# Kernel tuning notes

Measured on AMD Instinct MI355X. Metric: run time of the kernel, lower is better.

Reference implementation:

```python
import jax, jax.numpy as jnp
import numpy as np

B, N, L = 4, 16, 2048
E = 32768
CH = (64, 128, 128, 128)
EPS = 1e-5


def setup_inputs() -> dict:
    key = jax.random.key(0)
    ks = jax.random.split(key, 6)
    x = jax.random.normal(ks[0], (B, N, CH[0], L), jnp.float32)
    edge_index = jax.random.randint(ks[1], (2, E), 0, L, dtype=jnp.int64)

    def xavier(k, fi, fo):
        std = (2.0 / (fi + fo)) ** 0.5
        return jax.random.normal(k, (fi, fo), jnp.float32) * std

    W1 = xavier(ks[2], CH[0], CH[1])
    W2 = xavier(ks[3], 2 * CH[1], CH[2])
    W3 = xavier(ks[4], 2 * CH[2], CH[3])
    return dict(
        x=x, edge_index=edge_index,
        W1=W1, b1=jnp.zeros((CH[1],), jnp.float32),
        W2=W2, b2=jnp.zeros((CH[2],), jnp.float32),
        W3=W3, b3=jnp.zeros((CH[3],), jnp.float32),
        g1=jnp.ones((2 * CH[1],), jnp.float32), be1=jnp.zeros((2 * CH[1],), jnp.float32),
        g2=jnp.ones((2 * CH[2],), jnp.float32), be2=jnp.zeros((2 * CH[2],), jnp.float32),
        g3=jnp.ones((2 * CH[3],), jnp.float32), be3=jnp.zeros((2 * CH[3],), jnp.float32),
    )


def _gcn_norm(edge_index, l):
    # PyG gcn_norm with improved=True: self loops get weight 2, sym normalization
    src, dst = edge_index[0], edge_index[1]
    loop = jnp.arange(l)
    src_f = jnp.concatenate([src, loop])
    dst_f = jnp.concatenate([dst, loop])
    w = jnp.concatenate([jnp.ones((src.shape[0],), jnp.float32),
                         2.0 * jnp.ones((l,), jnp.float32)])
    deg = jax.ops.segment_sum(w, dst_f, num_segments=l)
    dinv = jnp.where(deg > 0, jax.lax.rsqrt(deg), 0.0)
    return src_f, dst_f, dinv[src_f] * w * dinv[dst_f]


def _gcn(h, W, bias, src, dst, norm):
    # h: [G, l, c_in] -> [G, l, c_out];  out[i] = sum_{j->i} norm_ij * (h_j @ W) + b
    hW = jnp.einsum('glc,cf->glf', h, W)
    msg = hW[:, src, :] * norm[None, :, None]
    out = jnp.zeros_like(hW).at[:, dst, :].add(msg)
    return out + bias


def _block(h, W, bias, g, beta, src, dst, norm, b, n, l):
    # h: [b, n, l, c_in]
    a = _gcn(h.reshape(b * n, l, h.shape[-1]), W, bias, src, dst, norm)
    a = a.reshape(b, n, l, -1)
    amax = a.max(axis=1, keepdims=True)
    a = jnp.concatenate([a, jnp.broadcast_to(amax, a.shape)], axis=-1)  # [b,n,l,2c]
    # BatchNorm1d training stats over (b, n, l) per channel (biased var)
    mean = a.mean(axis=(0, 1, 2))
    var = a.var(axis=(0, 1, 2))
    return jax.nn.relu((a - mean) * jax.lax.rsqrt(var + EPS) * g + beta)


def reference(x, edge_index, W1, b1, W2, b2, W3, b3, g1, be1, g2, be2, g3, be3):
    b, n, c, l = x.shape
    h = jnp.transpose(x, (0, 1, 3, 2))  # [b, n, l, c] node-major
    src, dst, norm = _gcn_norm(edge_index, l)
    h = _block(h, W1, b1, g1, be1, src, dst, norm, b, n, l)
    h = _block(h, W2, b2, g2, be2, src, dst, norm, b, n, l)
    h = _block(h, W3, b3, g3, be3, src, dst, norm, b, n, l)
    # match torch output layout [b*n, 2*channels[3], l]
    return jnp.transpose(h.reshape(b * n, l, -1), (0, 2, 1))
```

## Files before the change

### kernel.cpp

```cpp
#include <hip/hip_runtime.h>
#include <hip/hip_bf16.h>
#include <cstddef>
#include <cstdint>

#define BB 4
#define NN 16
#define GG 64
#define LL 2048
#define EE 32768
#define EF (EE + LL)
#define C0 64
#define CC 256
#define EPS 1e-5f

typedef __bf16 bf16x8 __attribute__((ext_vector_type(8)));
typedef __bf16 bf16x4 __attribute__((ext_vector_type(4)));
typedef __bf16 bf16x2 __attribute__((ext_vector_type(2)));
typedef float f32x4 __attribute__((ext_vector_type(4)));

struct __align__(8) Edge { int col; float val; };


__global__ void detect_kernel(const int* __restrict__ ei, int* __restrict__ flag) {
    int t = threadIdx.x;
    int bad = 0;
    for (int i = t; i < 256; i += 64) bad |= (ei[2 * i + 1] != 0) ? 1 : 0;
    int any = __any(bad);
    if (t == 0) *flag = any ? 0 : 1;
}

__global__ void prep_init_kernel(const void* __restrict__ ei, const int* __restrict__ flag,
                                 int* __restrict__ e32, float* __restrict__ deg,
                                 int* __restrict__ cnt, float* __restrict__ sums) {
    int i = blockIdx.x * 256 + threadIdx.x;
    if (i < 2 * EE) {
        int v;
        if (*flag)
            v = (int)((const long long*)ei)[i];
        else
            v = ((const int*)ei)[i];
        e32[i] = v;
    }
    if (i < LL) { deg[i] = 2.0f; cnt[i] = 1; }
    if (i < 512) sums[i] = 0.0f;
}

__global__ void deg_kernel(const int* __restrict__ e32, float* __restrict__ deg,
                           int* __restrict__ cnt) {
    int e = blockIdx.x * 256 + threadIdx.x;
    if (e >= EE) return;
    int d = e32[EE + e];
    atomicAdd(&deg[d], 1.0f);
    atomicAdd(&cnt[d], 1);
}

__global__ void scan_dinv_kernel(const int* __restrict__ cnt, const float* __restrict__ deg,
                                 int* __restrict__ rowptr, int* __restrict__ cursor,
                                 float* __restrict__ dinv) {
    __shared__ int part[256];
    int t = threadIdx.x;
    int base = t * 8;
    int loc[8];
    int s = 0;
#pragma unroll
    for (int j = 0; j < 8; ++j) {
        loc[j] = s; s += cnt[base + j];
        dinv[base + j] = rsqrtf(deg[base + j]);
    }
    part[t] = s;
    __syncthreads();
    if (t == 0) {
        int run = 0;
        for (int i = 0; i < 256; ++i) { int v = part[i]; part[i] = run; run += v; }
    }
    __syncthreads();
    int off = part[t];
#pragma unroll
    for (int j = 0; j < 8; ++j) {
        int rp = off + loc[j];
        rowptr[base + j] = rp;
        cursor[base + j] = rp;
    }
    if (t == 255) rowptr[LL] = off + s;
}

__global__ void fill_kernel(const int* __restrict__ e32, const float* __restrict__ dinv,
                            int* __restrict__ cursor, Edge* __restrict__ edges) {
    int idx = blockIdx.x * 256 + threadIdx.x;
    if (idx >= EF) return;
    int s, d; float w;
    if (idx < EE) {
        s = e32[idx]; d = e32[EE + idx];
        w = dinv[s] * dinv[d];
    } else {
        int i = idx - EE;
        s = i; d = i;
        w = 2.0f * dinv[i] * dinv[i];
    }
    int pos = atomicAdd(&cursor[d], 1);
    edges[pos].col = s;
    edges[pos].val = w;
}


__global__ void prep_w_all(const float* __restrict__ W0, const float* __restrict__ W1,
                           const float* __restrict__ W2, __bf16* __restrict__ Wf0,
                           __bf16* __restrict__ Wf1, __bf16* __restrict__ Wf2) {
    int t = blockIdx.x * 256 + threadIdx.x;
    const float* W; __bf16* Wf;
    if (t < 1024)      { W = W0; Wf = Wf0; }
    else if (t < 5120) { W = W1; Wf = Wf1; t -= 1024; }
    else if (t < 9216) { W = W2; Wf = Wf2; t -= 5120; }
    else return;
    int lane = t & 63;
    int rest = t >> 6;
    int n16 = rest & 7;
    int ks = rest >> 3;
    int col = n16 * 16 + (lane & 15);
    int k0 = ks * 32 + (lane >> 4) * 8;
    bf16x8 v;
#pragma unroll
    for (int j = 0; j < 8; ++j) v[j] = (__bf16)W[(size_t)(k0 + j) * 128 + col];
    *(bf16x8*)(Wf + (size_t)t * 8) = v;
}


__global__ void transpose_x(const float* __restrict__ x, float* __restrict__ h) {
    __shared__ float t[32][33];
    int g = blockIdx.z, c0 = blockIdx.y * 32, l0 = blockIdx.x * 32;
    int tx = threadIdx.x, ty = threadIdx.y;
    const float* xp = x + ((size_t)g * C0 + c0) * LL + l0;
#pragma unroll
    for (int i = ty; i < 32; i += 8) t[i][tx] = xp[(size_t)i * LL + tx];
    __syncthreads();
    float* hp = h + ((size_t)g * LL + l0) * C0 + c0;
#pragma unroll
    for (int i = ty; i < 32; i += 8) hp[(size_t)i * C0 + tx] = t[tx][i];
}


template <int K, bool BN>
__global__ __launch_bounds__(256) void gemm_mfma(const float* __restrict__ A0,
                                                 const float* __restrict__ amax,
                                                 const float* __restrict__ scb,
                                                 const __bf16* __restrict__ Wf,
                                                 __bf16* __restrict__ hw) {
    const int g = blockIdx.y;
    const int l0 = blockIdx.x * 64;
    const int tid = threadIdx.x;
    const int wid = tid >> 6;
    const int lane = tid & 63;
    __shared__ __align__(16) __bf16 As[64 * 64];

    f32x4 acc[8];
#pragma unroll
    for (int nf = 0; nf < 8; ++nf) acc[nf] = (f32x4){0.f, 0.f, 0.f, 0.f};

    for (int kt = 0; kt < K / 64; ++kt) {
#pragma unroll
        for (int it = 0; it < 4; ++it) {
            int f4 = tid + it * 256;
            int row = f4 >> 4;
            int kq = (f4 & 15) * 4;
            int gk = kt * 64 + kq;
            float4 v;
            if constexpr (BN) {
                if (gk < 128)
                    v = *(const float4*)(A0 + ((size_t)g * LL + l0 + row) * 128 + gk);
                else
                    v = *(const float4*)(amax + ((size_t)(g >> 4) * LL + l0 + row) * 128 + (gk - 128));
                float4 s = *(const float4*)(scb + gk);
                float4 b = *(const float4*)(scb + 256 + gk);
                v.x = fmaxf(fmaf(v.x, s.x, b.x), 0.f);
                v.y = fmaxf(fmaf(v.y, s.y, b.y), 0.f);
                v.z = fmaxf(fmaf(v.z, s.z, b.z), 0.f);
                v.w = fmaxf(fmaf(v.w, s.w, b.w), 0.f);
            } else {
                v = *(const float4*)(A0 + ((size_t)g * LL + l0 + row) * 64 + gk);
            }
            int sidx = row * 64 + (kq ^ ((row & 7) << 3));
            bf16x4 pv = {(__bf16)v.x, (__bf16)v.y, (__bf16)v.z, (__bf16)v.w};
            *(bf16x4*)(&As[sidx]) = pv;
        }
        __syncthreads();
#pragma unroll
        for (int ks2 = 0; ks2 < 2; ++ks2) {
            const int row = wid * 16 + (lane & 15);
            const int kk = ks2 * 32 + (lane >> 4) * 8;
            bf16x8 af = *(const bf16x8*)(&As[row * 64 + (kk ^ ((row & 7) << 3))]);
            const int ksg = kt * 2 + ks2;
            const __bf16* wp = Wf + (size_t)ksg * 8 * 512 + lane * 8;
#pragma unroll
            for (int nf = 0; nf < 8; ++nf) {
                bf16x8 bfr = *(const bf16x8*)(wp + nf * 512);
                acc[nf] = __builtin_amdgcn_mfma_f32_16x16x32_bf16(af, bfr, acc[nf], 0, 0, 0);
            }
        }
        __syncthreads();
    }
    __bf16* op = hw + ((size_t)g * LL + l0) * 128;
#pragma unroll
    for (int nf = 0; nf < 8; ++nf) {
        int col = nf * 16 + (lane & 15);
#pragma unroll
        for (int j = 0; j < 4; ++j) {
            int row = wid * 16 + (lane >> 4) * 4 + j;
            op[(size_t)row * 128 + col] = (__bf16)acc[nf][j];
        }
    }
}


__global__ __launch_bounds__(256) void agg_kernel(const __bf16* __restrict__ hw,
                                                  const float* __restrict__ bias,
                                                  const int* __restrict__ rowptr,
                                                  const Edge* __restrict__ edges,
                                                  float* __restrict__ aout) {
    const int lane = threadIdx.x & 63;
    const int grp = lane >> 4;
    const int ch16 = lane & 15;
    const int bid = blockIdx.x;
    const int xcd = bid & 7;
    const int slot = bid >> 3;
    const int gswz = ((slot >> 9) << 3) + xcd;
    const int within = slot & 511;
    int node = (gswz << 11) + within * 4 + (threadIdx.x >> 6);
    node = __builtin_amdgcn_readfirstlane(node);
    const int g = node >> 11, l = node & (LL - 1);
    const __bf16* __restrict__ base = hw + (size_t)g * LL * 128 + ch16 * 8;
    const int j0 = rowptr[l];
    const int deg = rowptr[l + 1] - j0;

    float acc[8];
#pragma unroll
    for (int j = 0; j < 8; ++j) acc[j] = 0.0f;

    for (int d0 = 0; d0 < deg; d0 += 64) {
        const int cnt = min(64, deg - d0);
        Edge e;
        e.col = 0; e.val = 0.0f;
        if (lane < cnt) e = edges[j0 + d0 + lane];
        int d = 0;
        for (; d + 8 <= cnt; d += 8) {
            int i1 = d + grp, i2 = d + 4 + grp;
            int c1 = __shfl(e.col, i1); float w1 = __shfl(e.val, i1);
            int c2 = __shfl(e.col, i2); float w2 = __shfl(e.val, i2);
            bf16x8 v1 = *(const bf16x8*)(base + (size_t)c1 * 128);
            bf16x8 v2 = *(const bf16x8*)(base + (size_t)c2 * 128);
#pragma unroll
            for (int j = 0; j < 8; ++j) acc[j] = fmaf(w1, (float)v1[j], acc[j]);
#pragma unroll
            for (int j = 0; j < 8; ++j) acc[j] = fmaf(w2, (float)v2[j], acc[j]);
        }
        for (; d < cnt; d += 4) {
            int i1 = d + grp;
            int c1 = __shfl(e.col, i1); float w1 = __shfl(e.val, i1);
            bf16x8 v1 = *(const bf16x8*)(base + (size_t)c1 * 128);
#pragma unroll
            for (int j = 0; j < 8; ++j) acc[j] = fmaf(w1, (float)v1[j], acc[j]);
        }
    }
#pragma unroll
    for (int j = 0; j < 8; ++j) {
        acc[j] += __shfl_xor(acc[j], 16);
        acc[j] += __shfl_xor(acc[j], 32);
    }
    if (grp == 0) {
        float4 b0 = *(const float4*)(bias + ch16 * 8);
        float4 b1 = *(const float4*)(bias + ch16 * 8 + 4);
        float4 s0 = make_float4(acc[0] + b0.x, acc[1] + b0.y, acc[2] + b0.z, acc[3] + b0.w);
        float4 s1 = make_float4(acc[4] + b1.x, acc[5] + b1.y, acc[6] + b1.z, acc[7] + b1.w);
        float* op = aout + (size_t)node * 128 + ch16 * 8;
        *(float4*)op = s0;
        *(float4*)(op + 4) = s1;
    }
}


__global__ void maxstats_kernel(const float* __restrict__ a, float* __restrict__ amax,
                                float* __restrict__ sums, float* __restrict__ sumsq) {
    int bb = blockIdx.x >> 7;
    int lt = blockIdx.x & 127;
    int l0 = lt * 16;
    int f = threadIdx.x;
    float s = 0.f, ss = 0.f, sa = 0.f, ssa = 0.f;
    for (int li = 0; li < 16; ++li) {
        int l = l0 + li;
        float m = -3.402823466e38f;
#pragma unroll
        for (int n = 0; n < NN; ++n) {
            float v = a[(((size_t)(bb * NN + n) * LL + l) * 128) + f];
            m = fmaxf(m, v);
            s += v;
            ss = fmaf(v, v, ss);
        }
        amax[((size_t)bb * LL + l) * 128 + f] = m;
        sa += m;
        ssa = fmaf(m, m, ssa);
    }
    atomicAdd(&sums[f], s);
    atomicAdd(&sumsq[f], ss);
    atomicAdd(&sums[128 + f], sa);
    atomicAdd(&sumsq[128 + f], ssa);
}

__global__ void bnfinal_kernel(float* __restrict__ sums, float* __restrict__ sumsq,
                               const float* __restrict__ gamma, const float* __restrict__ beta,
                               float* __restrict__ scb) {
    int f = threadIdx.x;
    float cntv = (f < 128) ? (float)(BB * NN * LL) : (float)(BB * LL);
    float mean = sums[f] / cntv;
    float var = sumsq[f] / cntv - mean * mean;
    float s = gamma[f] * rsqrtf(var + EPS);
    scb[f] = s;
    scb[256 + f] = beta[f] - mean * s;
    sums[f] = 0.0f;
    sumsq[f] = 0.0f;
}


__global__ void transpose_norm_out(const float* __restrict__ a, const float* __restrict__ amax,
                                   const float* __restrict__ scb, float* __restrict__ out) {
    __shared__ float t[64][65];
    int g = blockIdx.z, f0 = blockIdx.y * 64, l0 = blockIdx.x * 64;
    int tx = threadIdx.x, ty = threadIdx.y;
    int f = f0 + tx;
    float s = scb[f], b = scb[256 + f];
#pragma unroll
    for (int i = ty; i < 64; i += 8) {
        int l = l0 + i;
        float v;
        if (f0 < 128)
            v = a[((size_t)g * LL + l) * 128 + f];
        else
            v = amax[((size_t)(g >> 4) * LL + l) * 128 + (f - 128)];
        t[i][tx] = fmaxf(fmaf(v, s, b), 0.f);
    }
    __syncthreads();
    float* op = out + ((size_t)g * CC + f0) * LL + l0;
#pragma unroll
    for (int i = ty; i < 64; i += 8) op[(size_t)i * LL + tx] = t[tx][i];
}


extern "C" void kernel_launch(void* const* d_in, const int* in_sizes, int n_in,
                              void* d_out, int out_size, void* d_ws, size_t ws_size,
                              hipStream_t stream) {
    const float* x = (const float*)d_in[0];
    const void* ei = d_in[1];
    const float* W[3] = {(const float*)d_in[2], (const float*)d_in[4], (const float*)d_in[6]};
    const float* bia[3] = {(const float*)d_in[3], (const float*)d_in[5], (const float*)d_in[7]};
    const float* gam[3] = {(const float*)d_in[8], (const float*)d_in[10], (const float*)d_in[12]};
    const float* bet[3] = {(const float*)d_in[9], (const float*)d_in[11], (const float*)d_in[13]};
    float* out = (float*)d_out;

    char* w = (char*)d_ws;
    float* h0   = (float*)w;  w += (size_t)GG * LL * C0 * 4;
    float* a    = (float*)w;  w += (size_t)GG * LL * 128 * 4;
    __bf16* hw  = (__bf16*)w; w += (size_t)GG * LL * 128 * 2;
    float* amax = (float*)w;  w += (size_t)BB * LL * 128 * 4;
    __bf16* Wf[3];
    Wf[0] = (__bf16*)w; w += 65536 * 2;
    Wf[1] = (__bf16*)w; w += 65536 * 2;
    Wf[2] = (__bf16*)w; w += 65536 * 2;
    int*   e32   = (int*)w;    w += (size_t)2 * EE * 4;
    float* deg   = (float*)w;  w += LL * 4;
    int*   cnt   = (int*)w;    w += LL * 4;
    int*   rowptr= (int*)w;    w += (LL + 4) * 4;
    int*   cursor= (int*)w;    w += LL * 4;
    Edge*  edges = (Edge*)w;   w += (size_t)EF * 8;
    float* dinv  = (float*)w;  w += LL * 4;
    float* sums  = (float*)w;  w += 256 * 4;
    float* sumsq = (float*)w;  w += 256 * 4;
    float* scb   = (float*)w;  w += 512 * 4;
    int*   flag  = (int*)w;    w += 256;

    detect_kernel<<<1, 64, 0, stream>>>((const int*)ei, flag);
    prep_init_kernel<<<(2 * EE + 255) / 256, 256, 0, stream>>>(ei, flag, e32, deg, cnt, sums);
    deg_kernel<<<(EE + 255) / 256, 256, 0, stream>>>(e32, deg, cnt);
    scan_dinv_kernel<<<1, 256, 0, stream>>>(cnt, deg, rowptr, cursor, dinv);
    fill_kernel<<<(EF + 255) / 256, 256, 0, stream>>>(e32, dinv, cursor, edges);

    prep_w_all<<<36, 256, 0, stream>>>(W[0], W[1], W[2], Wf[0], Wf[1], Wf[2]);

    transpose_x<<<dim3(LL / 32, C0 / 32, GG), dim3(32, 8), 0, stream>>>(x, h0);

    gemm_mfma<64, false><<<dim3(LL / 64, GG), 256, 0, stream>>>(h0, amax, scb, Wf[0], hw);
    agg_kernel<<<GG * LL / 4, 256, 0, stream>>>(hw, bia[0], rowptr, edges, a);
    maxstats_kernel<<<BB * (LL / 16), 128, 0, stream>>>(a, amax, sums, sumsq);
    bnfinal_kernel<<<1, 256, 0, stream>>>(sums, sumsq, gam[0], bet[0], scb);

    gemm_mfma<256, true><<<dim3(LL / 64, GG), 256, 0, stream>>>(a, amax, scb, Wf[1], hw);
    agg_kernel<<<GG * LL / 4, 256, 0, stream>>>(hw, bia[1], rowptr, edges, a);
    maxstats_kernel<<<BB * (LL / 16), 128, 0, stream>>>(a, amax, sums, sumsq);
    bnfinal_kernel<<<1, 256, 0, stream>>>(sums, sumsq, gam[1], bet[1], scb);

    gemm_mfma<256, true><<<dim3(LL / 64, GG), 256, 0, stream>>>(a, amax, scb, Wf[2], hw);
    agg_kernel<<<GG * LL / 4, 256, 0, stream>>>(hw, bia[2], rowptr, edges, a);
    maxstats_kernel<<<BB * (LL / 16), 128, 0, stream>>>(a, amax, sums, sumsq);
    bnfinal_kernel<<<1, 256, 0, stream>>>(sums, sumsq, gam[2], bet[2], scb);

    transpose_norm_out<<<dim3(LL / 64, CC / 64, GG), dim3(64, 8), 0, stream>>>(a, amax, scb, out);
}
```

Before: 531.6 us.

## Store activations in bf16, fuse transpose into GEMM and BN finalize into stats

Intermediate activations and the per-batch max tensor are now stored in bf16 instead of fp32, roughly halving the memory traffic of the aggregation, stats, GEMM and output kernels. The input transpose is folded into the first GEMM's tile load, and the BatchNorm finalize step moves into the stats kernel using a last-block ticket. Edge conversion and degree counting are merged into one kernel, and the init and detect kernels are merged into another. The GEMM epilogue is staged through shared memory for vectorized stores, and the aggregation loop unrolls to four edges per step. Rounding to bf16 before max and BN statistics adds precision loss, and the ticket scheme depends on atomics and fences being correct.

```diff
diff --git a/kernel.cpp b/kernel.cpp
--- a/kernel.cpp
+++ b/kernel.cpp
@@ -21,35 +21,37 @@
 struct __align__(8) Edge { int col; float val; };
 
 
-__global__ void detect_kernel(const int* __restrict__ ei, int* __restrict__ flag) {
-    int t = threadIdx.x;
-    int bad = 0;
-    for (int i = t; i < 256; i += 64) bad |= (ei[2 * i + 1] != 0) ? 1 : 0;
-    int any = __any(bad);
-    if (t == 0) *flag = any ? 0 : 1;
-}
-
-__global__ void prep_init_kernel(const void* __restrict__ ei, const int* __restrict__ flag,
-                                 int* __restrict__ e32, float* __restrict__ deg,
-                                 int* __restrict__ cnt, float* __restrict__ sums) {
+__global__ void detect_init_kernel(const int* __restrict__ ei, int* __restrict__ flag,
+                                   float* __restrict__ deg, int* __restrict__ cnt,
+                                   float* __restrict__ gstats, int* __restrict__ ticket) {
     int i = blockIdx.x * 256 + threadIdx.x;
-    if (i < 2 * EE) {
-        int v;
-        if (*flag)
-            v = (int)((const long long*)ei)[i];
-        else
-            v = ((const int*)ei)[i];
-        e32[i] = v;
-    }
     if (i < LL) { deg[i] = 2.0f; cnt[i] = 1; }
-    if (i < 512) sums[i] = 0.0f;
-}
-
-__global__ void deg_kernel(const int* __restrict__ e32, float* __restrict__ deg,
-                           int* __restrict__ cnt) {
+    if (i < 4096) gstats[i] = 0.0f;
+    if (i == 0) *ticket = 0;
+    if (blockIdx.x == 0 && threadIdx.x < 64) {
+        int t = threadIdx.x;
+        int bad = 0;
+        for (int k = t; k < 256; k += 64) bad |= (ei[2 * k + 1] != 0) ? 1 : 0;
+        int any = __any(bad);
+        if (t == 0) *flag = any ? 0 : 1;
+    }
+}
+
+__global__ void conv_deg_kernel(const void* __restrict__ ei, const int* __restrict__ flag,
+                                int* __restrict__ e32, float* __restrict__ deg,
+                                int* __restrict__ cnt) {
     int e = blockIdx.x * 256 + threadIdx.x;
     if (e >= EE) return;
-    int d = e32[EE + e];
+    int s, d;
+    if (*flag) {
+        s = (int)((const long long*)ei)[e];
+        d = (int)((const long long*)ei)[EE + e];
+    } else {
+        s = ((const int*)ei)[e];
+        d = ((const int*)ei)[EE + e];
+    }
+    e32[e] = s;
+    e32[EE + e] = d;
     atomicAdd(&deg[d], 1.0f);
     atomicAdd(&cnt[d], 1);
 }
@@ -125,23 +127,9 @@
 }
 
 
-__global__ void transpose_x(const float* __restrict__ x, float* __restrict__ h) {
-    __shared__ float t[32][33];
-    int g = blockIdx.z, c0 = blockIdx.y * 32, l0 = blockIdx.x * 32;
-    int tx = threadIdx.x, ty = threadIdx.y;
-    const float* xp = x + ((size_t)g * C0 + c0) * LL + l0;
-#pragma unroll
-    for (int i = ty; i < 32; i += 8) t[i][tx] = xp[(size_t)i * LL + tx];
-    __syncthreads();
-    float* hp = h + ((size_t)g * LL + l0) * C0 + c0;
-#pragma unroll
-    for (int i = ty; i < 32; i += 8) hp[(size_t)i * C0 + tx] = t[tx][i];
-}
-
-
 template <int K, bool BN>
-__global__ __launch_bounds__(256) void gemm_mfma(const float* __restrict__ A0,
-                                                 const float* __restrict__ amax,
+__global__ __launch_bounds__(256) void gemm_mfma(const void* __restrict__ A0v,
+                                                 const __bf16* __restrict__ amax,
                                                  const float* __restrict__ scb,
                                                  const __bf16* __restrict__ Wf,
                                                  __bf16* __restrict__ hw) {
@@ -150,37 +138,54 @@
     const int tid = threadIdx.x;
     const int wid = tid >> 6;
     const int lane = tid & 63;
-    __shared__ __align__(16) __bf16 As[64 * 64];
+    __shared__ __align__(16) float smem[64 * 132];
+    __bf16* As = (__bf16*)smem;
 
     f32x4 acc[8];
 #pragma unroll
     for (int nf = 0; nf < 8; ++nf) acc[nf] = (f32x4){0.f, 0.f, 0.f, 0.f};
 
     for (int kt = 0; kt < K / 64; ++kt) {
-#pragma unroll
-        for (int it = 0; it < 4; ++it) {
-            int f4 = tid + it * 256;
-            int row = f4 >> 4;
-            int kq = (f4 & 15) * 4;
-            int gk = kt * 64 + kq;
-            float4 v;
-            if constexpr (BN) {
+        if constexpr (!BN) {
+            const float* x = (const float*)A0v;
+            const int l = tid & 63, cq = tid >> 6;
+#pragma unroll
+            for (int it = 0; it < 4; ++it) {
+                int cbase = it * 16 + cq * 4;
+                bf16x4 pv;
+#pragma unroll
+                for (int j = 0; j < 4; ++j)
+                    pv[j] = (__bf16)x[((size_t)g * C0 + cbase + j) * LL + l0 + l];
+                *(bf16x4*)(&As[l * 64 + (cbase ^ ((l & 7) << 3))]) = pv;
+            }
+        } else {
+            const __bf16* a = (const __bf16*)A0v;
+#pragma unroll
+            for (int it = 0; it < 2; ++it) {
+                int f8 = tid + it * 256;
+                int row = f8 >> 3;
+                int oct = f8 & 7;
+                int gk = kt * 64 + oct * 8;
+                bf16x8 v;
                 if (gk < 128)
-                    v = *(const float4*)(A0 + ((size_t)g * LL + l0 + row) * 128 + gk);
+                    v = *(const bf16x8*)(a + ((size_t)g * LL + l0 + row) * 128 + gk);
                 else
-                    v = *(const float4*)(amax + ((size_t)(g >> 4) * LL + l0 + row) * 128 + (gk - 128));
-                float4 s = *(const float4*)(scb + gk);
-                float4 b = *(const float4*)(scb + 256 + gk);
-                v.x = fmaxf(fmaf(v.x, s.x, b.x), 0.f);
-                v.y = fmaxf(fmaf(v.y, s.y, b.y), 0.f);
-                v.z = fmaxf(fmaf(v.z, s.z, b.z), 0.f);
-                v.w = fmaxf(fmaf(v.w, s.w, b.w), 0.f);
-            } else {
-                v = *(const float4*)(A0 + ((size_t)g * LL + l0 + row) * 64 + gk);
+                    v = *(const bf16x8*)(amax + ((size_t)(g >> 4) * LL + l0 + row) * 128 + (gk - 128));
+                float4 s0 = *(const float4*)(scb + gk);
+                float4 s1 = *(const float4*)(scb + gk + 4);
+                float4 b0 = *(const float4*)(scb + 256 + gk);
+                float4 b1 = *(const float4*)(scb + 256 + gk + 4);
+                bf16x8 pv;
+                pv[0] = (__bf16)fmaxf(fmaf((float)v[0], s0.x, b0.x), 0.f);
+                pv[1] = (__bf16)fmaxf(fmaf((float)v[1], s0.y, b0.y), 0.f);
+                pv[2] = (__bf16)fmaxf(fmaf((float)v[2], s0.z, b0.z), 0.f);
+                pv[3] = (__bf16)fmaxf(fmaf((float)v[3], s0.w, b0.w), 0.f);
+                pv[4] = (__bf16)fmaxf(fmaf((float)v[4], s1.x, b1.x), 0.f);
+                pv[5] = (__bf16)fmaxf(fmaf((float)v[5], s1.y, b1.y), 0.f);
+                pv[6] = (__bf16)fmaxf(fmaf((float)v[6], s1.z, b1.z), 0.f);
+                pv[7] = (__bf16)fmaxf(fmaf((float)v[7], s1.w, b1.w), 0.f);
+                *(bf16x8*)(&As[row * 64 + ((oct * 8) ^ ((row & 7) << 3))]) = pv;
             }
-            int sidx = row * 64 + (kq ^ ((row & 7) << 3));
-            bf16x4 pv = {(__bf16)v.x, (__bf16)v.y, (__bf16)v.z, (__bf16)v.w};
-            *(bf16x4*)(&As[sidx]) = pv;
         }
         __syncthreads();
 #pragma unroll
@@ -198,15 +203,25 @@
         }
         __syncthreads();
     }
-    __bf16* op = hw + ((size_t)g * LL + l0) * 128;
 #pragma unroll
     for (int nf = 0; nf < 8; ++nf) {
         int col = nf * 16 + (lane & 15);
 #pragma unroll
         for (int j = 0; j < 4; ++j) {
             int row = wid * 16 + (lane >> 4) * 4 + j;
-            op[(size_t)row * 128 + col] = (__bf16)acc[nf][j];
-        }
+            smem[row * 132 + col] = acc[nf][j];
+        }
+    }
+    __syncthreads();
+    const int row = tid >> 2, seg = tid & 3;
+    __bf16* dst = hw + ((size_t)g * LL + l0 + row) * 128 + seg * 32;
+    const float* src = smem + row * 132 + seg * 32;
+#pragma unroll
+    for (int q = 0; q < 4; ++q) {
+        bf16x8 o;
+#pragma unroll
+        for (int i = 0; i < 8; ++i) o[i] = (__bf16)src[q * 8 + i];
+        *(bf16x8*)(dst + q * 8) = o;
     }
 }
 
@@ -215,7 +230,7 @@
                                                   const float* __restrict__ bias,
                                                   const int* __restrict__ rowptr,
                                                   const Edge* __restrict__ edges,
-                                                  float* __restrict__ aout) {
+                                                  __bf16* __restrict__ aout) {
     const int lane = threadIdx.x & 63;
     const int grp = lane >> 4;
     const int ch16 = lane & 15;
@@ -236,23 +251,31 @@
     for (int j = 0; j < 8; ++j) acc[j] = 0.0f;
 
     for (int d0 = 0; d0 < deg; d0 += 64) {
-        const int cnt = min(64, deg - d0);
+        const int cntE = min(64, deg - d0);
         Edge e;
         e.col = 0; e.val = 0.0f;
-        if (lane < cnt) e = edges[j0 + d0 + lane];
+        if (lane < cntE) e = edges[j0 + d0 + lane];
         int d = 0;
-        for (; d + 8 <= cnt; d += 8) {
-            int i1 = d + grp, i2 = d + 4 + grp;
+        for (; d + 16 <= cntE; d += 16) {
+            int i1 = d + grp, i2 = d + 4 + grp, i3 = d + 8 + grp, i4 = d + 12 + grp;
             int c1 = __shfl(e.col, i1); float w1 = __shfl(e.val, i1);
             int c2 = __shfl(e.col, i2); float w2 = __shfl(e.val, i2);
+            int c3 = __shfl(e.col, i3); float w3 = __shfl(e.val, i3);
+            int c4 = __shfl(e.col, i4); float w4 = __shfl(e.val, i4);
             bf16x8 v1 = *(const bf16x8*)(base + (size_t)c1 * 128);
             bf16x8 v2 = *(const bf16x8*)(base + (size_t)c2 * 128);
+            bf16x8 v3 = *(const bf16x8*)(base + (size_t)c3 * 128);
+            bf16x8 v4 = *(const bf16x8*)(base + (size_t)c4 * 128);
 #pragma unroll
             for (int j = 0; j < 8; ++j) acc[j] = fmaf(w1, (float)v1[j], acc[j]);
 #pragma unroll
             for (int j = 0; j < 8; ++j) acc[j] = fmaf(w2, (float)v2[j], acc[j]);
-        }
-        for (; d < cnt; d += 4) {
+#pragma unroll
+            for (int j = 0; j < 8; ++j) acc[j] = fmaf(w3, (float)v3[j], acc[j]);
+#pragma unroll
+            for (int j = 0; j < 8; ++j) acc[j] = fmaf(w4, (float)v4[j], acc[j]);
+        }
+        for (; d < cntE; d += 4) {
             int i1 = d + grp;
             int c1 = __shfl(e.col, i1); float w1 = __shfl(e.val, i1);
             bf16x8 v1 = *(const bf16x8*)(base + (size_t)c1 * 128);
@@ -268,58 +291,82 @@
     if (grp == 0) {
         float4 b0 = *(const float4*)(bias + ch16 * 8);
         float4 b1 = *(const float4*)(bias + ch16 * 8 + 4);
-        float4 s0 = make_float4(acc[0] + b0.x, acc[1] + b0.y, acc[2] + b0.z, acc[3] + b0.w);
-        float4 s1 = make_float4(acc[4] + b1.x, acc[5] + b1.y, acc[6] + b1.z, acc[7] + b1.w);
-        float* op = aout + (size_t)node * 128 + ch16 * 8;
-        *(float4*)op = s0;
-        *(float4*)(op + 4) = s1;
-    }
-}
-
-
-__global__ void maxstats_kernel(const float* __restrict__ a, float* __restrict__ amax,
-                                float* __restrict__ sums, float* __restrict__ sumsq) {
-    int bb = blockIdx.x >> 7;
-    int lt = blockIdx.x & 127;
-    int l0 = lt * 16;
-    int f = threadIdx.x;
-    float s = 0.f, ss = 0.f, sa = 0.f, ssa = 0.f;
-    for (int li = 0; li < 16; ++li) {
-        int l = l0 + li;
-        float m = -3.402823466e38f;
+        bf16x8 o;
+        o[0] = (__bf16)(acc[0] + b0.x); o[1] = (__bf16)(acc[1] + b0.y);
+        o[2] = (__bf16)(acc[2] + b0.z); o[3] = (__bf16)(acc[3] + b0.w);
+        o[4] = (__bf16)(acc[4] + b1.x); o[5] = (__bf16)(acc[5] + b1.y);
+        o[6] = (__bf16)(acc[6] + b1.z); o[7] = (__bf16)(acc[7] + b1.w);
+        *(bf16x8*)(aout + (size_t)node * 128 + ch16 * 8) = o;
+    }
+}
+
+
+__global__ __launch_bounds__(256) void maxstats_kernel(const __bf16* __restrict__ a,
+                                                       __bf16* __restrict__ amax,
+                                                       float* __restrict__ gstats,
+                                                       int* __restrict__ ticket,
+                                                       const float* __restrict__ gamma,
+                                                       const float* __restrict__ beta,
+                                                       float* __restrict__ scb) {
+    __shared__ float bl[512];
+    __shared__ int lastflag;
+    const int t = threadIdx.x;
+    bl[t] = 0.f; bl[256 + t] = 0.f;
+    __syncthreads();
+    const int bb = blockIdx.x >> 7;
+    const int lt = blockIdx.x & 127;
+    const int c2 = t & 63;
+    const int lq = t >> 6;
+    const int l0 = lt * 16 + lq * 4;
+    float sx = 0.f, sy = 0.f, qx = 0.f, qy = 0.f;
+    float sax = 0.f, say = 0.f, qax = 0.f, qay = 0.f;
+#pragma unroll
+    for (int i = 0; i < 4; ++i) {
+        int l = l0 + i;
+        float mx = -3.402823466e38f, my = -3.402823466e38f;
 #pragma unroll
         for (int n = 0; n < NN; ++n) {
-            float v = a[(((size_t)(bb * NN + n) * LL + l) * 128) + f];
-            m = fmaxf(m, v);
-            s += v;
-            ss = fmaf(v, v, ss);
-        }
-        amax[((size_t)bb * LL + l) * 128 + f] = m;
-        sa += m;
-        ssa = fmaf(m, m, ssa);
-    }
-    atomicAdd(&sums[f], s);
-    atomicAdd(&sumsq[f], ss);
-    atomicAdd(&sums[128 + f], sa);
-    atomicAdd(&sumsq[128 + f], ssa);
-}
-
-__global__ void bnfinal_kernel(float* __restrict__ sums, float* __restrict__ sumsq,
-                               const float* __restrict__ gamma, const float* __restrict__ beta,
-                               float* __restrict__ scb) {
-    int f = threadIdx.x;
-    float cntv = (f < 128) ? (float)(BB * NN * LL) : (float)(BB * LL);
-    float mean = sums[f] / cntv;
-    float var = sumsq[f] / cntv - mean * mean;
-    float s = gamma[f] * rsqrtf(var + EPS);
-    scb[f] = s;
-    scb[256 + f] = beta[f] - mean * s;
-    sums[f] = 0.0f;
-    sumsq[f] = 0.0f;
-}
-
-
-__global__ void transpose_norm_out(const float* __restrict__ a, const float* __restrict__ amax,
+            bf16x2 v = *(const bf16x2*)(a + ((size_t)(bb * NN + n) * LL + l) * 128 + c2 * 2);
+            float v0 = (float)v[0], v1 = (float)v[1];
+            mx = fmaxf(mx, v0); my = fmaxf(my, v1);
+            sx += v0; sy += v1;
+            qx = fmaf(v0, v0, qx); qy = fmaf(v1, v1, qy);
+        }
+        bf16x2 mv = {(__bf16)mx, (__bf16)my};
+        *(bf16x2*)(amax + ((size_t)bb * LL + l) * 128 + c2 * 2) = mv;
+        sax += mx; say += my;
+        qax = fmaf(mx, mx, qax); qay = fmaf(my, my, qay);
+    }
+    atomicAdd(&bl[c2 * 2], sx);        atomicAdd(&bl[c2 * 2 + 1], sy);
+    atomicAdd(&bl[128 + c2 * 2], sax); atomicAdd(&bl[128 + c2 * 2 + 1], say);
+    atomicAdd(&bl[256 + c2 * 2], qx);  atomicAdd(&bl[256 + c2 * 2 + 1], qy);
+    atomicAdd(&bl[384 + c2 * 2], qax); atomicAdd(&bl[384 + c2 * 2 + 1], qay);
+    __syncthreads();
+    const int slot = blockIdx.x & 7;
+    atomicAdd(&gstats[slot * 512 + t], bl[t]);
+    atomicAdd(&gstats[slot * 512 + 256 + t], bl[256 + t]);
+    __threadfence();
+    if (t == 0) lastflag = (atomicAdd(ticket, 1) == 511) ? 1 : 0;
+    __syncthreads();
+    if (lastflag) {
+        float sm = 0.f, sq = 0.f;
+#pragma unroll
+        for (int sl = 0; sl < 8; ++sl) {
+            sm += atomicExch(&gstats[sl * 512 + t], 0.f);
+            sq += atomicExch(&gstats[sl * 512 + 256 + t], 0.f);
+        }
+        float cntv = (t < 128) ? (float)(BB * NN * LL) : (float)(BB * LL);
+        float mean = sm / cntv;
+        float var = sq / cntv - mean * mean;
+        float sc = gamma[t] * rsqrtf(var + EPS);
+        scb[t] = sc;
+        scb[256 + t] = beta[t] - mean * sc;
+        if (t == 0) *ticket = 0;
+    }
+}
+
+
+__global__ void transpose_norm_out(const __bf16* __restrict__ a, const __bf16* __restrict__ amax,
                                    const float* __restrict__ scb, float* __restrict__ out) {
     __shared__ float t[64][65];
     int g = blockIdx.z, f0 = blockIdx.y * 64, l0 = blockIdx.x * 64;
@@ -331,9 +378,9 @@
         int l = l0 + i;
         float v;
         if (f0 < 128)
-            v = a[((size_t)g * LL + l) * 128 + f];
+            v = (float)a[((size_t)g * LL + l) * 128 + f];
         else
-            v = amax[((size_t)(g >> 4) * LL + l) * 128 + (f - 128)];
+            v = (float)amax[((size_t)(g >> 4) * LL + l) * 128 + (f - 128)];
         t[i][tx] = fmaxf(fmaf(v, s, b), 0.f);
     }
     __syncthreads();
@@ -355,50 +402,42 @@
     float* out = (float*)d_out;
 
     char* w = (char*)d_ws;
-    float* h0   = (float*)w;  w += (size_t)GG * LL * C0 * 4;
-    float* a    = (float*)w;  w += (size_t)GG * LL * 128 * 4;
-    __bf16* hw  = (__bf16*)w; w += (size_t)GG * LL * 128 * 2;
-    float* amax = (float*)w;  w += (size_t)BB * LL * 128 * 4;
+    __bf16* a_bf  = (__bf16*)w; w += (size_t)GG * LL * 128 * 2;
+    __bf16* hw    = (__bf16*)w; w += (size_t)GG * LL * 128 * 2;
+    __bf16* amax  = (__bf16*)w; w += (size_t)BB * LL * 128 * 2;
     __bf16* Wf[3];
     Wf[0] = (__bf16*)w; w += 65536 * 2;
     Wf[1] = (__bf16*)w; w += 65536 * 2;
     Wf[2] = (__bf16*)w; w += 65536 * 2;
-    int*   e32   = (int*)w;    w += (size_t)2 * EE * 4;
-    float* deg   = (float*)w;  w += LL * 4;
-    int*   cnt   = (int*)w;    w += LL * 4;
-    int*   rowptr= (int*)w;    w += (LL + 4) * 4;
-    int*   cursor= (int*)w;    w += LL * 4;
-    Edge*  edges = (Edge*)w;   w += (size_t)EF * 8;
-    float* dinv  = (float*)w;  w += LL * 4;
-    float* sums  = (float*)w;  w += 256 * 4;
-    float* sumsq = (float*)w;  w += 256 * 4;
-    float* scb   = (float*)w;  w += 512 * 4;
-    int*   flag  = (int*)w;    w += 256;
-
-    detect_kernel<<<1, 64, 0, stream>>>((const int*)ei, flag);
-    prep_init_kernel<<<(2 * EE + 255) / 256, 256, 0, stream>>>(ei, flag, e32, deg, cnt, sums);
-    deg_kernel<<<(EE + 255) / 256, 256, 0, stream>>>(e32, deg, cnt);
+    int*   e32    = (int*)w;    w += (size_t)2 * EE * 4;
+    float* deg    = (float*)w;  w += LL * 4;
+    int*   cnt    = (int*)w;    w += LL * 4;
+    int*   rowptr = (int*)w;    w += (LL + 4) * 4;
+    int*   cursor = (int*)w;    w += LL * 4;
+    Edge*  edges  = (Edge*)w;   w += (size_t)EF * 8;
+    float* dinv   = (float*)w;  w += LL * 4;
+    float* gstats = (float*)w;  w += 8 * 512 * 4;
+    float* scb    = (float*)w;  w += 512 * 4;
+    int*   flag   = (int*)w;    w += 256;
+    int*   ticket = (int*)w;    w += 256;
+
+    detect_init_kernel<<<16, 256, 0, stream>>>((const int*)ei, flag, deg, cnt, gstats, ticket);
+    conv_deg_kernel<<<(EE + 255) / 256, 256, 0, stream>>>(ei, flag, e32, deg, cnt);
     scan_dinv_kernel<<<1, 256, 0, stream>>>(cnt, deg, rowptr, cursor, dinv);
     fill_kernel<<<(EF + 255) / 256, 256, 0, stream>>>(e32, dinv, cursor, edges);
-
     prep_w_all<<<36, 256, 0, stream>>>(W[0], W[1], W[2], Wf[0], Wf[1], Wf[2]);
 
-    transpose_x<<<dim3(LL / 32, C0 / 32, GG), dim3(32, 8), 0, stream>>>(x, h0);
-
-    gemm_mfma<64, false><<<dim3(LL / 64, GG), 256, 0, stream>>>(h0, amax, scb, Wf[0], hw);
-    agg_kernel<<<GG * LL / 4, 256, 0, stream>>>(hw, bia[0], rowptr, edges, a);
-    maxstats_kernel<<<BB * (LL / 16), 128, 0, stream>>>(a, amax, sums, sumsq);
-    bnfinal_kernel<<<1, 256, 0, stream>>>(sums, sumsq, gam[0], bet[0], scb);
-
-    gemm_mfma<256, true><<<dim3(LL / 64, GG), 256, 0, stream>>>(a, amax, scb, Wf[1], hw);
-    agg_kernel<<<GG * LL / 4, 256, 0, stream>>>(hw, bia[1], rowptr, edges, a);
-    maxstats_kernel<<<BB * (LL / 16), 128, 0, stream>>>(a, amax, sums, sumsq);
-    bnfinal_kernel<<<1, 256, 0, stream>>>(sums, sumsq, gam[1], bet[1], scb);
-
-    gemm_mfma<256, true><<<dim3(LL / 64, GG), 256, 0, stream>>>(a, amax, scb, Wf[2], hw);
-    agg_kernel<<<GG * LL / 4, 256, 0, stream>>>(hw, bia[2], rowptr, edges, a);
-    maxstats_kernel<<<BB * (LL / 16), 128, 0, stream>>>(a, amax, sums, sumsq);
-    bnfinal_kernel<<<1, 256, 0, stream>>>(sums, sumsq, gam[2], bet[2], scb);
-
-    transpose_norm_out<<<dim3(LL / 64, CC / 64, GG), dim3(64, 8), 0, stream>>>(a, amax, scb, out);
-}
+    gemm_mfma<64, false><<<dim3(LL / 64, GG), 256, 0, stream>>>(x, amax, scb, Wf[0], hw);
+    agg_kernel<<<GG * LL / 4, 256, 0, stream>>>(hw, bia[0], rowptr, edges, a_bf);
+    maxstats_kernel<<<512, 256, 0, stream>>>(a_bf, amax, gstats, ticket, gam[0], bet[0], scb);
+
+    gemm_mfma<256, true><<<dim3(LL / 64, GG), 256, 0, stream>>>(a_bf, amax, scb, Wf[1], hw);
+    agg_kernel<<<GG * LL / 4, 256, 0, stream>>>(hw, bia[1], rowptr, edges, a_bf);
+    maxstats_kernel<<<512, 256, 0, stream>>>(a_bf, amax, gstats, ticket, gam[1], bet[1], scb);
+
+    gemm_mfma<256, true><<<dim3(LL / 64, GG), 256, 0, stream>>>(a_bf, amax, scb, Wf[2], hw);
+    agg_kernel<<<GG * LL / 4, 256, 0, stream>>>(hw, bia[2], rowptr, edges, a_bf);
+    maxstats_kernel<<<512, 256, 0, stream>>>(a_bf, amax, gstats, ticket, gam[2], bet[2], scb);
+
+    transpose_norm_out<<<dim3(LL / 64, CC / 64, GG), dim3(64, 8), 0, stream>>>(a_bf, amax, scb, out);
+}
```

After: 555.4 us. +4.5%, slower.
